# Performance work log

Hardware: AMD Instinct MI355X
Metric: run time of the kernel (lower is better)

## Reference

```python
import jax, jax.numpy as jnp
import numpy as np

N_NODES = 250000
N_EDGES = 5000000


def setup_inputs() -> dict:
    key = jax.random.key(0)
    k1, k2, k3, k4, k5, k6 = jax.random.split(key, 6)
    x = jax.random.normal(k1, (N_NODES, 1), dtype=jnp.float32)
    edge_index = jax.random.randint(k2, (2, N_EDGES), 0, N_NODES, dtype=jnp.int64)
    # Glorot-style small weights like PyG GCNConv init
    W1 = jax.random.normal(k3, (1, 16), dtype=jnp.float32) * (1.0 / np.sqrt(1 + 16))
    b1 = jnp.zeros((16,), dtype=jnp.float32)
    W2 = jax.random.normal(k4, (16, 2), dtype=jnp.float32) * (1.0 / np.sqrt(16 + 2))
    b2 = jnp.zeros((2,), dtype=jnp.float32)
    return {"x": x, "edge_index": edge_index, "W1": W1, "b1": b1, "W2": W2, "b2": b2}


def _gcn_conv(x, row, col, W, b, n_nodes):
    """PyG GCNConv: x' = D^{-1/2} (A + I) D^{-1/2} (x W) + b.

    row = source nodes, col = target nodes (messages flow row -> col).
    Self-loops are assumed already appended to row/col.
    """
    h = x @ W  # [N, out]
    ones = jnp.ones(row.shape[0], dtype=h.dtype)
    deg = jax.ops.segment_sum(ones, col, num_segments=n_nodes)  # in-degree incl. self-loop
    dinv = jnp.where(deg > 0, jax.lax.rsqrt(deg), 0.0)
    norm = dinv[row] * dinv[col]  # [E+N]
    msg = h[row] * norm[:, None]  # gather + scale  [E+N, out]
    out = jax.ops.segment_sum(msg, col, num_segments=n_nodes)  # scatter-add
    return out + b


def reference(x, edge_index, W1, b1, W2, b2):
    n = x.shape[0]
    loop = jnp.arange(n, dtype=edge_index.dtype)
    row = jnp.concatenate([edge_index[0], loop])
    col = jnp.concatenate([edge_index[1], loop])
    h = _gcn_conv(x, row, col, W1, b1, n)
    h = jax.nn.relu(h)
    # F.dropout(training=False) at inference -> identity
    h = _gcn_conv(h, row, col, W2, b2, n)
    return jax.nn.softmax(h, axis=1)
```

## Files before the change

kernel.cpp:

```cpp
#include <hip/hip_runtime.h>

#define ST 512
#define PT 24
#define EPB (ST * PT)
#define CSHIFT 10
#define CMASK 1023u
#define CW 1024
#define NCMAX 255
#define CAP 24576


__global__ void k_init(unsigned* __restrict__ gcur, int NC) {
    for (int b = threadIdx.x; b < NC; b += blockDim.x)
        gcur[b] = (unsigned)b * CAP;
}

__global__ __launch_bounds__(ST) void k_sortk(const int* __restrict__ row,
                                              const int* __restrict__ col,
                                              unsigned* __restrict__ gcur,
                                              unsigned* __restrict__ pack1,
                                              int E, int NC) {
    __shared__ unsigned loff[NCMAX + 2];
    __shared__ unsigned gbase[NCMAX + 1];
    __shared__ unsigned cur[NCMAX + 1];
    __shared__ unsigned staging[EPB];

    const int t = threadIdx.x;
    for (int i = t; i <= NC; i += ST) loff[i] = 0;
    __syncthreads();

    const int base = blockIdx.x * EPB;
    int c[PT];

#pragma unroll
    for (int k = 0; k < PT / 4; ++k) {
        int e = base + (k * ST + t) * 4;
        int4 cc;
        if (e + 3 < E) {
            cc = *reinterpret_cast<const int4*>(col + e);
        } else {
            cc.x = (e     < E) ? col[e]     : -1;
            cc.y = (e + 1 < E) ? col[e + 1] : -1;
            cc.z = (e + 2 < E) ? col[e + 2] : -1;
            cc.w = (e + 3 < E) ? col[e + 3] : -1;
        }
        c[4 * k] = cc.x; c[4 * k + 1] = cc.y; c[4 * k + 2] = cc.z; c[4 * k + 3] = cc.w;
    }
#pragma unroll
    for (int k = 0; k < PT; ++k)
        if (c[k] >= 0) atomicAdd(&loff[((unsigned)c[k] >> CSHIFT) + 1], 1u);
    __syncthreads();

    if (t < 64) {
        unsigned v[4];
        unsigned ls = 0;
#pragma unroll
        for (int k = 0; k < 4; ++k) {
            int idx = t * 4 + k;
            v[k] = (idx <= NC) ? loff[idx] : 0;
            ls += v[k];
        }
        unsigned sc = ls;
#pragma unroll
        for (int d = 1; d < 64; d <<= 1) {
            unsigned n = __shfl_up(sc, d, 64);
            if (t >= d) sc += n;
        }
        unsigned run = sc - ls;
#pragma unroll
        for (int k = 0; k < 4; ++k) {
            int idx = t * 4 + k;
            run += v[k];
            if (idx <= NC) loff[idx] = run;
        }
    }
    __syncthreads();

    if (t < NC) {
        unsigned cb = loff[t + 1] - loff[t];
        gbase[t] = atomicAdd(&gcur[t], cb);
        cur[t] = loff[t];
    }
    __syncthreads();

#pragma unroll
    for (int k = 0; k < PT / 4; ++k) {
        int e = base + (k * ST + t) * 4;
        int4 rr = make_int4(0, 0, 0, 0);
        if (e + 3 < E) {
            rr = *reinterpret_cast<const int4*>(row + e);
        } else {
            rr.x = (e     < E) ? row[e]     : 0;
            rr.y = (e + 1 < E) ? row[e + 1] : 0;
            rr.z = (e + 2 < E) ? row[e + 2] : 0;
            rr.w = (e + 3 < E) ? row[e + 3] : 0;
        }
        int rl[4] = {rr.x, rr.y, rr.z, rr.w};
#pragma unroll
        for (int j = 0; j < 4; ++j) {
            int cc = c[4 * k + j];
            if (cc >= 0) {
                unsigned b = (unsigned)cc >> CSHIFT;
                unsigned p = atomicAdd(&cur[b], 1u);
                staging[p] = ((unsigned)rl[j] << CSHIFT) | ((unsigned)cc & CMASK);
            }
        }
    }
    __syncthreads();

    const int wave = t >> 6;
    const int lane = t & 63;
    for (int b = wave; b < NC; b += ST / 64) {
        unsigned lo = loff[b];
        unsigned hi = loff[b + 1];
        unsigned gb = gbase[b];
        unsigned lim = (unsigned)(b + 1) * CAP;
        for (unsigned i = lo + lane; i < hi; i += 64) {
            unsigned pos = gb + (i - lo);
            if (pos < lim)
                pack1[pos] = staging[i];
        }
    }
}


__global__ __launch_bounds__(CW) void k_degk(const unsigned* __restrict__ pack1,
                                             const unsigned* __restrict__ gcur,
                                             const float* __restrict__ x,
                                             float* __restrict__ dinv, float* __restrict__ xs,
                                             int N) {
    __shared__ unsigned dcnt[CW];
    const int b = blockIdx.x;
    const int t = threadIdx.x;
    dcnt[t] = 0;
    __syncthreads();
    unsigned s0 = (unsigned)b * CAP;
    unsigned s1 = min(gcur[b], s0 + (unsigned)CAP);
    unsigned n4 = (s1 - s0) >> 2;
    for (unsigned i = t; i < n4; i += CW) {
        uint4 p = reinterpret_cast<const uint4*>(pack1 + s0)[i];
        atomicAdd(&dcnt[p.x & CMASK], 1u);
        atomicAdd(&dcnt[p.y & CMASK], 1u);
        atomicAdd(&dcnt[p.z & CMASK], 1u);
        atomicAdd(&dcnt[p.w & CMASK], 1u);
    }
    unsigned i = s0 + (n4 << 2) + t;
    if (i < s1) atomicAdd(&dcnt[pack1[i] & CMASK], 1u);
    __syncthreads();
    int v = (b << CSHIFT) + t;
    if (v < N) {
        float di = rsqrtf((float)dcnt[t] + 1.0f);
        dinv[v] = di;
        xs[v] = di * x[v];
    }
}

__global__ __launch_bounds__(CW) void k_l1k(const unsigned* __restrict__ pack1,
                                            const unsigned* __restrict__ gcur,
                                            const float* __restrict__ xs,
                                            const float* __restrict__ dinv,
                                            const float* __restrict__ W1,
                                            const float* __restrict__ b1,
                                            const float* __restrict__ W2,
                                            float* __restrict__ gs, int N) {
    __shared__ float acc[CW];
    const int b = blockIdx.x;
    const int t = threadIdx.x;
    acc[t] = 0.0f;
    __syncthreads();
    unsigned s0 = (unsigned)b * CAP;
    unsigned s1 = min(gcur[b], s0 + (unsigned)CAP);
    unsigned n4 = (s1 - s0) >> 2;
    for (unsigned i = t; i < n4; i += CW) {
        uint4 p = reinterpret_cast<const uint4*>(pack1 + s0)[i];
        float v0 = xs[p.x >> CSHIFT];
        float v1 = xs[p.y >> CSHIFT];
        float v2 = xs[p.z >> CSHIFT];
        float v3 = xs[p.w >> CSHIFT];
        atomicAdd(&acc[p.x & CMASK], v0);
        atomicAdd(&acc[p.y & CMASK], v1);
        atomicAdd(&acc[p.z & CMASK], v2);
        atomicAdd(&acc[p.w & CMASK], v3);
    }
    unsigned i = s0 + (n4 << 2) + t;
    if (i < s1) {
        unsigned p = pack1[i];
        atomicAdd(&acc[p & CMASK], xs[p >> CSHIFT]);
    }
    __syncthreads();
    int v = (b << CSHIFT) + t;
    if (v < N) {
        float di = dinv[v];
        float tt = di * (acc[t] + xs[v]);
        float g = 0.0f;
#pragma unroll
        for (int jj = 0; jj < 16; ++jj) {
            float y = fmaxf(fmaf(W1[jj], tt, b1[jj]), 0.0f);
            g = fmaf(W2[2 * jj] - W2[2 * jj + 1], y, g);
        }
        gs[v] = di * g;
    }
}

__global__ __launch_bounds__(CW) void k_l2k(const unsigned* __restrict__ pack1,
                                            const unsigned* __restrict__ gcur,
                                            const float* __restrict__ gs,
                                            const float* __restrict__ dinv,
                                            const float* __restrict__ b2,
                                            float* __restrict__ out, int N) {
    __shared__ float acc[CW];
    const int b = blockIdx.x;
    const int t = threadIdx.x;
    acc[t] = 0.0f;
    __syncthreads();
    unsigned s0 = (unsigned)b * CAP;
    unsigned s1 = min(gcur[b], s0 + (unsigned)CAP);
    unsigned n4 = (s1 - s0) >> 2;
    for (unsigned i = t; i < n4; i += CW) {
        uint4 p = reinterpret_cast<const uint4*>(pack1 + s0)[i];
        float v0 = gs[p.x >> CSHIFT];
        float v1 = gs[p.y >> CSHIFT];
        float v2 = gs[p.z >> CSHIFT];
        float v3 = gs[p.w >> CSHIFT];
        atomicAdd(&acc[p.x & CMASK], v0);
        atomicAdd(&acc[p.y & CMASK], v1);
        atomicAdd(&acc[p.z & CMASK], v2);
        atomicAdd(&acc[p.w & CMASK], v3);
    }
    unsigned i = s0 + (n4 << 2) + t;
    if (i < s1) {
        unsigned p = pack1[i];
        atomicAdd(&acc[p & CMASK], gs[p >> CSHIFT]);
    }
    __syncthreads();
    int v = (b << CSHIFT) + t;
    if (v < N) {
        float diff = dinv[v] * (acc[t] + gs[v]) + (b2[0] - b2[1]);
        float p0 = 1.0f / (1.0f + __expf(-diff));
        float2 o;
        o.x = p0;
        o.y = 1.0f - p0;
        reinterpret_cast<float2*>(out)[v] = o;
    }
}

__global__ void k_zero_f(float* __restrict__ p, int n) {
    int i = blockIdx.x * blockDim.x + threadIdx.x;
    int v = i * 4;
    if (v + 3 < n) {
        reinterpret_cast<float4*>(p + v)[0] = make_float4(0.f, 0.f, 0.f, 0.f);
    } else {
        for (; v < n; ++v) p[v] = 0.0f;
    }
}
__global__ void k_deg_f(const int* __restrict__ col, float* __restrict__ deg, int E) {
    int i = blockIdx.x * blockDim.x + threadIdx.x;
    int e = i * 4;
    if (e + 3 < E) {
        int4 c = reinterpret_cast<const int4*>(col + e)[0];
        atomicAdd(deg + c.x, 1.0f); atomicAdd(deg + c.y, 1.0f);
        atomicAdd(deg + c.z, 1.0f); atomicAdd(deg + c.w, 1.0f);
    } else {
        for (; e < E; ++e) atomicAdd(deg + col[e], 1.0f);
    }
}
__global__ void k_node1_f(const float* __restrict__ x, float* __restrict__ degdinv,
                          float* __restrict__ xs, int N) {
    int v = blockIdx.x * blockDim.x + threadIdx.x;
    if (v < N) {
        float dinv = rsqrtf(degdinv[v] + 1.0f);
        degdinv[v] = dinv;
        xs[v] = dinv * x[v];
    }
}
__global__ void k_scat_f(const int* __restrict__ row, const int* __restrict__ col,
                         const float* __restrict__ src, float* __restrict__ acc, int E) {
    int i = blockIdx.x * blockDim.x + threadIdx.x;
    int e = i * 4;
    if (e + 3 < E) {
        int4 r = reinterpret_cast<const int4*>(row + e)[0];
        int4 c = reinterpret_cast<const int4*>(col + e)[0];
        float s0 = src[r.x], s1 = src[r.y], s2 = src[r.z], s3 = src[r.w];
        atomicAdd(acc + c.x, s0); atomicAdd(acc + c.y, s1);
        atomicAdd(acc + c.z, s2); atomicAdd(acc + c.w, s3);
    } else {
        for (; e < E; ++e) atomicAdd(acc + col[e], src[row[e]]);
    }
}
__global__ void k_mlp_f(const float* __restrict__ W1, const float* __restrict__ b1,
                        const float* __restrict__ W2, const float* __restrict__ dinv,
                        float* __restrict__ acc, float* __restrict__ xsgs, int N) {
    int v = blockIdx.x * blockDim.x + threadIdx.x;
    if (v < N) {
        float di = dinv[v];
        float t = di * (acc[v] + xsgs[v]);
        float g = 0.0f;
#pragma unroll
        for (int j = 0; j < 16; ++j) {
            float y = fmaxf(fmaf(W1[j], t, b1[j]), 0.0f);
            g = fmaf(W2[2 * j] - W2[2 * j + 1], y, g);
        }
        xsgs[v] = di * g;
        acc[v] = 0.0f;
    }
}
__global__ void k_out_f(const float* __restrict__ b2, const float* __restrict__ dinv,
                        const float* __restrict__ acc, const float* __restrict__ gs,
                        float* __restrict__ out, int N) {
    int v = blockIdx.x * blockDim.x + threadIdx.x;
    if (v < N) {
        float diff = dinv[v] * (acc[v] + gs[v]) + (b2[0] - b2[1]);
        float p0 = 1.0f / (1.0f + __expf(-diff));
        float2 o; o.x = p0; o.y = 1.0f - p0;
        reinterpret_cast<float2*>(out)[v] = o;
    }
}

extern "C" void kernel_launch(void* const* d_in, const int* in_sizes, int n_in,
                              void* d_out, int out_size, void* d_ws, size_t ws_size,
                              hipStream_t stream) {
    const float* x  = (const float*)d_in[0];
    const int* edge = (const int*)d_in[1];
    const float* W1 = (const float*)d_in[2];
    const float* b1 = (const float*)d_in[3];
    const float* W2 = (const float*)d_in[4];
    const float* b2 = (const float*)d_in[5];
    float* out = (float*)d_out;

    const int N = in_sizes[0];
    const int E = in_sizes[1] / 2;
    const int* row = edge;
    const int* col = edge + E;

    const int NC  = (N + CW - 1) >> CSHIFT;
    const int NBS = (E + EPB - 1) / EPB;

    const double mean = (double)E / NC;
    const double slack = mean + 8.0 * __builtin_sqrt(mean > 1.0 ? mean : 1.0);
    const size_t need = ((size_t)NC * CAP + NC) * 4 + (size_t)3 * N * 4;

    if (NC <= NCMAX && N < (1 << 22) && slack < CAP && ws_size >= need) {
        unsigned* pack1 = (unsigned*)d_ws;
        unsigned* gcur  = pack1 + (size_t)NC * CAP;
        float* dinv     = (float*)(gcur + NC);
        float* xs       = dinv + N;
        float* gs       = xs + N;

        k_init <<<1, 256, 0, stream>>>(gcur, NC);
        k_sortk<<<NBS, ST, 0, stream>>>(row, col, gcur, pack1, E, NC);
        k_degk <<<NC, CW, 0, stream>>>(pack1, gcur, x, dinv, xs, N);
        k_l1k  <<<NC, CW, 0, stream>>>(pack1, gcur, xs, dinv, W1, b1, W2, gs, N);
        k_l2k  <<<NC, CW, 0, stream>>>(pack1, gcur, gs, dinv, b2, out, N);
    } else {
        float* w0 = (float*)d_ws;
        float* w1 = w0 + N;
        float* w2 = w1 + N;
        const int nb = (N + 255) / 256;
        const int eb = ((E + 3) / 4 + 255) / 256;
        const int zb = ((2 * N + 3) / 4 + 255) / 256;
        k_zero_f <<<zb, 256, 0, stream>>>(w0, 2 * N);
        k_deg_f  <<<eb, 256, 0, stream>>>(col, w0, E);
        k_node1_f<<<nb, 256, 0, stream>>>(x, w0, w2, N);
        k_scat_f <<<eb, 256, 0, stream>>>(row, col, w2, w1, E);
        k_mlp_f  <<<nb, 256, 0, stream>>>(W1, b1, W2, w0, w1, w2, N);
        k_scat_f <<<eb, 256, 0, stream>>>(row, col, w2, w1, E);
        k_out_f  <<<nb, 256, 0, stream>>>(b2, w0, w1, w2, out, N);
    }
}
```

Baseline: 174.6 us.

## Sub-bucket edges by source slice and gather node values from LDS

Each destination bucket is split into 8 sub-buckets keyed by source-node slice. The sort kernel uses wave ballots to rank elements and reserve positions with per-sub-bucket atomics. The layer kernels then stage each 32K-node slice of xs/gs into 128KB of dynamic LDS and gather from shared memory instead of doing random global loads. The cost is extra ballot work in the sort, eight serial slice loads per block, scalar instead of uint4 edge loads, and much lower occupancy from the large LDS footprint.

```diff
diff --git a/kernel.cpp b/kernel.cpp
--- a/kernel.cpp
+++ b/kernel.cpp
@@ -1,18 +1,23 @@
 #include <hip/hip_runtime.h>
 
 #define ST 512
-#define PT 24
+#define PT 20
 #define EPB (ST * PT)
 #define CSHIFT 10
 #define CMASK 1023u
 #define CW 1024
 #define NCMAX 255
-#define CAP 24576
-
-
-__global__ void k_init(unsigned* __restrict__ gcur, int NC) {
-    for (int b = threadIdx.x; b < NC; b += blockDim.x)
-        gcur[b] = (unsigned)b * CAP;
+#define NS 8
+#define SSHIFT 15
+#define SMASK 32767u
+#define SLICE 32768
+#define SUBCAP 3072
+#define CAP (NS * SUBCAP)
+
+
+__global__ void k_init(unsigned* __restrict__ gcur, int NSB) {
+    for (int i = threadIdx.x; i < NSB; i += blockDim.x)
+        gcur[i] = (unsigned)i * SUBCAP;
 }
 
 __global__ __launch_bounds__(ST) void k_sortk(const int* __restrict__ row,
@@ -21,7 +26,6 @@
                                               unsigned* __restrict__ pack1,
                                               int E, int NC) {
     __shared__ unsigned loff[NCMAX + 2];
-    __shared__ unsigned gbase[NCMAX + 1];
     __shared__ unsigned cur[NCMAX + 1];
     __shared__ unsigned staging[EPB];
 
@@ -76,11 +80,7 @@
     }
     __syncthreads();
 
-    if (t < NC) {
-        unsigned cb = loff[t + 1] - loff[t];
-        gbase[t] = atomicAdd(&gcur[t], cb);
-        cur[t] = loff[t];
-    }
+    if (t < NC) cur[t] = loff[t];
     __syncthreads();
 
 #pragma unroll
@@ -110,15 +110,33 @@
 
     const int wave = t >> 6;
     const int lane = t & 63;
+    const unsigned long long lanemask_lt = (lane == 0) ? 0ull : ((~0ull) >> (64 - lane));
     for (int b = wave; b < NC; b += ST / 64) {
         unsigned lo = loff[b];
         unsigned hi = loff[b + 1];
-        unsigned gb = gbase[b];
-        unsigned lim = (unsigned)(b + 1) * CAP;
-        for (unsigned i = lo + lane; i < hi; i += 64) {
-            unsigned pos = gb + (i - lo);
-            if (pos < lim)
-                pack1[pos] = staging[i];
+        for (unsigned i0 = lo; i0 < hi; i0 += 64) {
+            unsigned i = i0 + lane;
+            bool valid = i < hi;
+            unsigned p = valid ? staging[i] : 0u;
+            unsigned sl = p >> (CSHIFT + SSHIFT);
+            unsigned long long mymask = 0;
+            unsigned cnt8 = 0;
+#pragma unroll
+            for (int s = 0; s < NS; ++s) {
+                unsigned long long m = __ballot(valid && sl == (unsigned)s);
+                if (valid && sl == (unsigned)s) mymask = m;
+                if (lane == s) cnt8 = (unsigned)__popcll(m);
+            }
+            unsigned rbase = 0;
+            if (lane < NS && cnt8)
+                rbase = atomicAdd(&gcur[b * NS + lane], cnt8);
+            unsigned mybase = __shfl(rbase, (int)sl, 64);
+            if (valid) {
+                unsigned rank = (unsigned)__popcll(mymask & lanemask_lt);
+                unsigned pos = mybase + rank;
+                if (pos < ((unsigned)b * NS + sl + 1u) * (unsigned)SUBCAP)
+                    pack1[pos] = p;
+            }
         }
     }
 }
@@ -134,18 +152,13 @@
     const int t = threadIdx.x;
     dcnt[t] = 0;
     __syncthreads();
-    unsigned s0 = (unsigned)b * CAP;
-    unsigned s1 = min(gcur[b], s0 + (unsigned)CAP);
-    unsigned n4 = (s1 - s0) >> 2;
-    for (unsigned i = t; i < n4; i += CW) {
-        uint4 p = reinterpret_cast<const uint4*>(pack1 + s0)[i];
-        atomicAdd(&dcnt[p.x & CMASK], 1u);
-        atomicAdd(&dcnt[p.y & CMASK], 1u);
-        atomicAdd(&dcnt[p.z & CMASK], 1u);
-        atomicAdd(&dcnt[p.w & CMASK], 1u);
-    }
-    unsigned i = s0 + (n4 << 2) + t;
-    if (i < s1) atomicAdd(&dcnt[pack1[i] & CMASK], 1u);
+    for (int s = 0; s < NS; ++s) {
+        unsigned sb = (unsigned)b * NS + s;
+        unsigned sbase = sb * SUBCAP;
+        unsigned cnt = min(gcur[sb] - sbase, (unsigned)SUBCAP);
+        for (unsigned i = t; i < cnt; i += CW)
+            atomicAdd(&dcnt[pack1[sbase + i] & CMASK], 1u);
+    }
     __syncthreads();
     int v = (b << CSHIFT) + t;
     if (v < N) {
@@ -154,6 +167,7 @@
         xs[v] = di * x[v];
     }
 }
+
 
 __global__ __launch_bounds__(CW) void k_l1k(const unsigned* __restrict__ pack1,
                                             const unsigned* __restrict__ gcur,
@@ -163,31 +177,31 @@
                                             const float* __restrict__ b1,
                                             const float* __restrict__ W2,
                                             float* __restrict__ gs, int N) {
+    extern __shared__ float sbuf[];
     __shared__ float acc[CW];
     const int b = blockIdx.x;
     const int t = threadIdx.x;
     acc[t] = 0.0f;
-    __syncthreads();
-    unsigned s0 = (unsigned)b * CAP;
-    unsigned s1 = min(gcur[b], s0 + (unsigned)CAP);
-    unsigned n4 = (s1 - s0) >> 2;
-    for (unsigned i = t; i < n4; i += CW) {
-        uint4 p = reinterpret_cast<const uint4*>(pack1 + s0)[i];
-        float v0 = xs[p.x >> CSHIFT];
-        float v1 = xs[p.y >> CSHIFT];
-        float v2 = xs[p.z >> CSHIFT];
-        float v3 = xs[p.w >> CSHIFT];
-        atomicAdd(&acc[p.x & CMASK], v0);
-        atomicAdd(&acc[p.y & CMASK], v1);
-        atomicAdd(&acc[p.z & CMASK], v2);
-        atomicAdd(&acc[p.w & CMASK], v3);
-    }
-    unsigned i = s0 + (n4 << 2) + t;
-    if (i < s1) {
-        unsigned p = pack1[i];
-        atomicAdd(&acc[p & CMASK], xs[p >> CSHIFT]);
-    }
-    __syncthreads();
+    const int n4 = N >> 2;
+    for (int s = 0; s < NS; ++s) {
+        const float4* x4 = reinterpret_cast<const float4*>(xs) + s * (SLICE / 4);
+        float4* b4 = reinterpret_cast<float4*>(sbuf);
+        const int lim = n4 - s * (SLICE / 4);
+#pragma unroll
+        for (int k = 0; k < SLICE / 4 / CW; ++k) {
+            int j = k * CW + t;
+            b4[j] = (j < lim) ? x4[j] : make_float4(0.f, 0.f, 0.f, 0.f);
+        }
+        __syncthreads();
+        unsigned sb = (unsigned)b * NS + s;
+        unsigned sbase = sb * SUBCAP;
+        unsigned cnt = min(gcur[sb] - sbase, (unsigned)SUBCAP);
+        for (unsigned i = t; i < cnt; i += CW) {
+            unsigned p = pack1[sbase + i];
+            atomicAdd(&acc[p & CMASK], sbuf[(p >> CSHIFT) & SMASK]);
+        }
+        __syncthreads();
+    }
     int v = (b << CSHIFT) + t;
     if (v < N) {
         float di = dinv[v];
@@ -208,31 +222,31 @@
                                             const float* __restrict__ dinv,
                                             const float* __restrict__ b2,
                                             float* __restrict__ out, int N) {
+    extern __shared__ float sbuf[];
     __shared__ float acc[CW];
     const int b = blockIdx.x;
     const int t = threadIdx.x;
     acc[t] = 0.0f;
-    __syncthreads();
-    unsigned s0 = (unsigned)b * CAP;
-    unsigned s1 = min(gcur[b], s0 + (unsigned)CAP);
-    unsigned n4 = (s1 - s0) >> 2;
-    for (unsigned i = t; i < n4; i += CW) {
-        uint4 p = reinterpret_cast<const uint4*>(pack1 + s0)[i];
-        float v0 = gs[p.x >> CSHIFT];
-        float v1 = gs[p.y >> CSHIFT];
-        float v2 = gs[p.z >> CSHIFT];
-        float v3 = gs[p.w >> CSHIFT];
-        atomicAdd(&acc[p.x & CMASK], v0);
-        atomicAdd(&acc[p.y & CMASK], v1);
-        atomicAdd(&acc[p.z & CMASK], v2);
-        atomicAdd(&acc[p.w & CMASK], v3);
-    }
-    unsigned i = s0 + (n4 << 2) + t;
-    if (i < s1) {
-        unsigned p = pack1[i];
-        atomicAdd(&acc[p & CMASK], gs[p >> CSHIFT]);
-    }
-    __syncthreads();
+    const int n4 = N >> 2;
+    for (int s = 0; s < NS; ++s) {
+        const float4* g4 = reinterpret_cast<const float4*>(gs) + s * (SLICE / 4);
+        float4* b4 = reinterpret_cast<float4*>(sbuf);
+        const int lim = n4 - s * (SLICE / 4);
+#pragma unroll
+        for (int k = 0; k < SLICE / 4 / CW; ++k) {
+            int j = k * CW + t;
+            b4[j] = (j < lim) ? g4[j] : make_float4(0.f, 0.f, 0.f, 0.f);
+        }
+        __syncthreads();
+        unsigned sb = (unsigned)b * NS + s;
+        unsigned sbase = sb * SUBCAP;
+        unsigned cnt = min(gcur[sb] - sbase, (unsigned)SUBCAP);
+        for (unsigned i = t; i < cnt; i += CW) {
+            unsigned p = pack1[sbase + i];
+            atomicAdd(&acc[p & CMASK], sbuf[(p >> CSHIFT) & SMASK]);
+        }
+        __syncthreads();
+    }
     int v = (b << CSHIFT) + t;
     if (v < N) {
         float diff = dinv[v] * (acc[t] + gs[v]) + (b2[0] - b2[1]);
@@ -333,24 +347,35 @@
     const int* col = edge + E;
 
     const int NC  = (N + CW - 1) >> CSHIFT;
+    const int NSB = NC * NS;
     const int NBS = (E + EPB - 1) / EPB;
 
-    const double mean = (double)E / NC;
-    const double slack = mean + 8.0 * __builtin_sqrt(mean > 1.0 ? mean : 1.0);
-    const size_t need = ((size_t)NC * CAP + NC) * 4 + (size_t)3 * N * 4;
-
-    if (NC <= NCMAX && N < (1 << 22) && slack < CAP && ws_size >= need) {
+    const double mean_sb = (double)E / ((double)NC * NS);
+    const double slack = mean_sb + 8.0 * __builtin_sqrt(mean_sb > 1.0 ? mean_sb : 1.0);
+    const size_t need = ((size_t)NC * CAP + NSB) * 4 + (size_t)3 * N * 4;
+
+    if (NC <= NCMAX && N <= NS * SLICE && (N & 3) == 0 && slack < SUBCAP &&
+        ws_size >= need) {
         unsigned* pack1 = (unsigned*)d_ws;
         unsigned* gcur  = pack1 + (size_t)NC * CAP;
-        float* dinv     = (float*)(gcur + NC);
+        float* dinv     = (float*)(gcur + NSB);
         float* xs       = dinv + N;
         float* gs       = xs + N;
 
-        k_init <<<1, 256, 0, stream>>>(gcur, NC);
+        static bool attr_done = false;
+        if (!attr_done) {
+            hipFuncSetAttribute((const void*)k_l1k,
+                                hipFuncAttributeMaxDynamicSharedMemorySize, SLICE * 4);
+            hipFuncSetAttribute((const void*)k_l2k,
+                                hipFuncAttributeMaxDynamicSharedMemorySize, SLICE * 4);
+            attr_done = true;
+        }
+
+        k_init <<<1, 256, 0, stream>>>(gcur, NSB);
         k_sortk<<<NBS, ST, 0, stream>>>(row, col, gcur, pack1, E, NC);
         k_degk <<<NC, CW, 0, stream>>>(pack1, gcur, x, dinv, xs, N);
-        k_l1k  <<<NC, CW, 0, stream>>>(pack1, gcur, xs, dinv, W1, b1, W2, gs, N);
-        k_l2k  <<<NC, CW, 0, stream>>>(pack1, gcur, gs, dinv, b2, out, N);
+        k_l1k  <<<NC, CW, SLICE * 4, stream>>>(pack1, gcur, xs, dinv, W1, b1, W2, gs, N);
+        k_l2k  <<<NC, CW, SLICE * 4, stream>>>(pack1, gcur, gs, dinv, b2, out, N);
     } else {
         float* w0 = (float*)d_ws;
         float* w1 = w0 + N;
```

New measurement: 275.1 us. 57.5% more time.

## Sub-sort buckets by source tile and gather layer features from LDS tiles

Applied to the files above, without the earlier changes.

Adds a per-destination-bucket counting sort, k_subk, that orders packed edges by 1024-node source tile. It records per-tile offsets in a new boff array and also computes degrees. Layer kernels now have each wave stage a 1024-node source tile of xs/gs into LDS, then gather from LDS instead of doing random global loads. The bucket cursor becomes a relative offset reset by a memset rather than an init kernel, and the sort's per-thread edge count drops. The cost is an extra read/write pass over the packed edges and a full 4 KB tile load for each non-empty (dst, src) tile pair, which may hold only a few dozen edges.

```diff
diff --git a/kernel.cpp b/kernel.cpp
--- a/kernel.cpp
+++ b/kernel.cpp
@@ -1,19 +1,15 @@
 #include <hip/hip_runtime.h>
 
 #define ST 512
-#define PT 24
+#define PT 20
 #define EPB (ST * PT)
 #define CSHIFT 10
 #define CMASK 1023u
 #define CW 1024
 #define NCMAX 255
 #define CAP 24576
-
-
-__global__ void k_init(unsigned* __restrict__ gcur, int NC) {
-    for (int b = threadIdx.x; b < NC; b += blockDim.x)
-        gcur[b] = (unsigned)b * CAP;
-}
+#define NWAVE (CW / 64)
+
 
 __global__ __launch_bounds__(ST) void k_sortk(const int* __restrict__ row,
                                               const int* __restrict__ col,
@@ -114,39 +110,78 @@
         unsigned lo = loff[b];
         unsigned hi = loff[b + 1];
         unsigned gb = gbase[b];
-        unsigned lim = (unsigned)(b + 1) * CAP;
         for (unsigned i = lo + lane; i < hi; i += 64) {
-            unsigned pos = gb + (i - lo);
-            if (pos < lim)
-                pack1[pos] = staging[i];
-        }
-    }
-}
-
-
-__global__ __launch_bounds__(CW) void k_degk(const unsigned* __restrict__ pack1,
+            unsigned off = gb + (i - lo);
+            if (off < CAP)
+                pack1[(unsigned)b * CAP + off] = staging[i];
+        }
+    }
+}
+
+
+__global__ __launch_bounds__(CW) void k_subk(unsigned* __restrict__ pack1,
                                              const unsigned* __restrict__ gcur,
                                              const float* __restrict__ x,
-                                             float* __restrict__ dinv, float* __restrict__ xs,
-                                             int N) {
+                                             float* __restrict__ dinv,
+                                             float* __restrict__ xs,
+                                             unsigned* __restrict__ boff,
+                                             int N, int NC) {
+    extern __shared__ unsigned sstage[];
+    __shared__ unsigned loff[NCMAX + 2];
+    __shared__ unsigned cur[NCMAX + 1];
     __shared__ unsigned dcnt[CW];
     const int b = blockIdx.x;
     const int t = threadIdx.x;
     dcnt[t] = 0;
-    __syncthreads();
-    unsigned s0 = (unsigned)b * CAP;
-    unsigned s1 = min(gcur[b], s0 + (unsigned)CAP);
-    unsigned n4 = (s1 - s0) >> 2;
-    for (unsigned i = t; i < n4; i += CW) {
-        uint4 p = reinterpret_cast<const uint4*>(pack1 + s0)[i];
-        atomicAdd(&dcnt[p.x & CMASK], 1u);
-        atomicAdd(&dcnt[p.y & CMASK], 1u);
-        atomicAdd(&dcnt[p.z & CMASK], 1u);
-        atomicAdd(&dcnt[p.w & CMASK], 1u);
-    }
-    unsigned i = s0 + (n4 << 2) + t;
-    if (i < s1) atomicAdd(&dcnt[pack1[i] & CMASK], 1u);
-    __syncthreads();
+    for (int i = t; i <= NC; i += CW) loff[i] = 0;
+    __syncthreads();
+
+    const unsigned s0 = (unsigned)b * CAP;
+    const unsigned cnt = min(gcur[b], (unsigned)CAP);
+
+    for (unsigned i = t; i < cnt; i += CW)
+        atomicAdd(&loff[(pack1[s0 + i] >> (CSHIFT + 10)) + 1], 1u);
+    __syncthreads();
+
+    if (t < 64) {
+        unsigned v[4];
+        unsigned ls = 0;
+#pragma unroll
+        for (int k = 0; k < 4; ++k) {
+            int idx = t * 4 + k;
+            v[k] = (idx <= NC) ? loff[idx] : 0;
+            ls += v[k];
+        }
+        unsigned sc = ls;
+#pragma unroll
+        for (int d = 1; d < 64; d <<= 1) {
+            unsigned n = __shfl_up(sc, d, 64);
+            if (t >= d) sc += n;
+        }
+        unsigned run = sc - ls;
+#pragma unroll
+        for (int k = 0; k < 4; ++k) {
+            int idx = t * 4 + k;
+            run += v[k];
+            if (idx <= NC) loff[idx] = run;
+        }
+    }
+    __syncthreads();
+    if (t <= NC) boff[(size_t)b * (NC + 1) + t] = loff[t];
+    if (t < NC) cur[t] = loff[t];
+    __syncthreads();
+
+    for (unsigned i = t; i < cnt; i += CW) {
+        unsigned p = pack1[s0 + i];
+        unsigned tile = p >> (CSHIFT + 10);
+        unsigned pos = atomicAdd(&cur[tile], 1u);
+        sstage[pos] = p;
+        atomicAdd(&dcnt[p & CMASK], 1u);
+    }
+    __syncthreads();
+
+    for (unsigned i = t; i < cnt; i += CW)
+        pack1[s0 + i] = sstage[i];
     int v = (b << CSHIFT) + t;
     if (v < N) {
         float di = rsqrtf((float)dcnt[t] + 1.0f);
@@ -155,37 +190,48 @@
     }
 }
 
+
 __global__ __launch_bounds__(CW) void k_l1k(const unsigned* __restrict__ pack1,
-                                            const unsigned* __restrict__ gcur,
+                                            const unsigned* __restrict__ boff,
                                             const float* __restrict__ xs,
                                             const float* __restrict__ dinv,
                                             const float* __restrict__ W1,
                                             const float* __restrict__ b1,
                                             const float* __restrict__ W2,
-                                            float* __restrict__ gs, int N) {
+                                            float* __restrict__ gs, int N, int NC) {
+    extern __shared__ float xtile[];
     __shared__ float acc[CW];
+    __shared__ unsigned bo[NCMAX + 2];
     const int b = blockIdx.x;
     const int t = threadIdx.x;
+    const int w = t >> 6;
+    const int lane = t & 63;
     acc[t] = 0.0f;
-    __syncthreads();
-    unsigned s0 = (unsigned)b * CAP;
-    unsigned s1 = min(gcur[b], s0 + (unsigned)CAP);
-    unsigned n4 = (s1 - s0) >> 2;
-    for (unsigned i = t; i < n4; i += CW) {
-        uint4 p = reinterpret_cast<const uint4*>(pack1 + s0)[i];
-        float v0 = xs[p.x >> CSHIFT];
-        float v1 = xs[p.y >> CSHIFT];
-        float v2 = xs[p.z >> CSHIFT];
-        float v3 = xs[p.w >> CSHIFT];
-        atomicAdd(&acc[p.x & CMASK], v0);
-        atomicAdd(&acc[p.y & CMASK], v1);
-        atomicAdd(&acc[p.z & CMASK], v2);
-        atomicAdd(&acc[p.w & CMASK], v3);
-    }
-    unsigned i = s0 + (n4 << 2) + t;
-    if (i < s1) {
-        unsigned p = pack1[i];
-        atomicAdd(&acc[p & CMASK], xs[p >> CSHIFT]);
+    if (t <= NC) bo[t] = boff[(size_t)b * (NC + 1) + t];
+    __syncthreads();
+
+    const unsigned s0 = (unsigned)b * CAP;
+    const int n44 = N >> 2;
+    const float4* x4 = reinterpret_cast<const float4*>(xs);
+    float4* tile4 = reinterpret_cast<float4*>(xtile + (w << 10));
+
+    for (int s = w; s < NC; s += NWAVE) {
+        unsigned off0 = bo[s];
+        unsigned off1 = bo[s + 1];
+        if (off0 == off1) continue;
+        int base4 = s << 8;
+#pragma unroll
+        for (int k = 0; k < 4; ++k) {
+            int q = lane + (k << 6);
+            int idx = base4 + q;
+            tile4[q] = (idx < n44) ? x4[idx] : make_float4(0.f, 0.f, 0.f, 0.f);
+        }
+        asm volatile("s_waitcnt lgkmcnt(0) vmcnt(0)" ::: "memory");
+        for (unsigned i = off0 + lane; i < off1; i += 64) {
+            unsigned p = pack1[s0 + i];
+            float val = xtile[(w << 10) | ((p >> CSHIFT) & CMASK)];
+            atomicAdd(&acc[p & CMASK], val);
+        }
     }
     __syncthreads();
     int v = (b << CSHIFT) + t;
@@ -203,34 +249,44 @@
 }
 
 __global__ __launch_bounds__(CW) void k_l2k(const unsigned* __restrict__ pack1,
-                                            const unsigned* __restrict__ gcur,
+                                            const unsigned* __restrict__ boff,
                                             const float* __restrict__ gs,
                                             const float* __restrict__ dinv,
                                             const float* __restrict__ b2,
-                                            float* __restrict__ out, int N) {
+                                            float* __restrict__ out, int N, int NC) {
+    extern __shared__ float xtile[];
     __shared__ float acc[CW];
+    __shared__ unsigned bo[NCMAX + 2];
     const int b = blockIdx.x;
     const int t = threadIdx.x;
+    const int w = t >> 6;
+    const int lane = t & 63;
     acc[t] = 0.0f;
-    __syncthreads();
-    unsigned s0 = (unsigned)b * CAP;
-    unsigned s1 = min(gcur[b], s0 + (unsigned)CAP);
-    unsigned n4 = (s1 - s0) >> 2;
-    for (unsigned i = t; i < n4; i += CW) {
-        uint4 p = reinterpret_cast<const uint4*>(pack1 + s0)[i];
-        float v0 = gs[p.x >> CSHIFT];
-        float v1 = gs[p.y >> CSHIFT];
-        float v2 = gs[p.z >> CSHIFT];
-        float v3 = gs[p.w >> CSHIFT];
-        atomicAdd(&acc[p.x & CMASK], v0);
-        atomicAdd(&acc[p.y & CMASK], v1);
-        atomicAdd(&acc[p.z & CMASK], v2);
-        atomicAdd(&acc[p.w & CMASK], v3);
-    }
-    unsigned i = s0 + (n4 << 2) + t;
-    if (i < s1) {
-        unsigned p = pack1[i];
-        atomicAdd(&acc[p & CMASK], gs[p >> CSHIFT]);
+    if (t <= NC) bo[t] = boff[(size_t)b * (NC + 1) + t];
+    __syncthreads();
+
+    const unsigned s0 = (unsigned)b * CAP;
+    const int n44 = N >> 2;
+    const float4* g4 = reinterpret_cast<const float4*>(gs);
+    float4* tile4 = reinterpret_cast<float4*>(xtile + (w << 10));
+
+    for (int s = w; s < NC; s += NWAVE) {
+        unsigned off0 = bo[s];
+        unsigned off1 = bo[s + 1];
+        if (off0 == off1) continue;
+        int base4 = s << 8;
+#pragma unroll
+        for (int k = 0; k < 4; ++k) {
+            int q = lane + (k << 6);
+            int idx = base4 + q;
+            tile4[q] = (idx < n44) ? g4[idx] : make_float4(0.f, 0.f, 0.f, 0.f);
+        }
+        asm volatile("s_waitcnt lgkmcnt(0) vmcnt(0)" ::: "memory");
+        for (unsigned i = off0 + lane; i < off1; i += 64) {
+            unsigned p = pack1[s0 + i];
+            float val = xtile[(w << 10) | ((p >> CSHIFT) & CMASK)];
+            atomicAdd(&acc[p & CMASK], val);
+        }
     }
     __syncthreads();
     int v = (b << CSHIFT) + t;
@@ -337,20 +393,38 @@
 
     const double mean = (double)E / NC;
     const double slack = mean + 8.0 * __builtin_sqrt(mean > 1.0 ? mean : 1.0);
-    const size_t need = ((size_t)NC * CAP + NC) * 4 + (size_t)3 * N * 4;
-
-    if (NC <= NCMAX && N < (1 << 22) && slack < CAP && ws_size >= need) {
+    const size_t need = ((size_t)NC * CAP + NC + (size_t)NC * (NC + 1)) * 4 +
+                        (size_t)3 * N * 4;
+
+    if (NC <= NCMAX && N < (1 << 22) && (N & 3) == 0 && slack < CAP &&
+        ws_size >= need) {
         unsigned* pack1 = (unsigned*)d_ws;
         unsigned* gcur  = pack1 + (size_t)NC * CAP;
-        float* dinv     = (float*)(gcur + NC);
+        unsigned* boff  = gcur + NC;
+        float* dinv     = (float*)(boff + (size_t)NC * (NC + 1));
         float* xs       = dinv + N;
         float* gs       = xs + N;
 
-        k_init <<<1, 256, 0, stream>>>(gcur, NC);
+        static bool attr_done = false;
+        if (!attr_done) {
+            hipFuncSetAttribute((const void*)k_subk,
+                                hipFuncAttributeMaxDynamicSharedMemorySize, CAP * 4);
+            hipFuncSetAttribute((const void*)k_l1k,
+                                hipFuncAttributeMaxDynamicSharedMemorySize,
+                                NWAVE * 1024 * 4);
+            hipFuncSetAttribute((const void*)k_l2k,
+                                hipFuncAttributeMaxDynamicSharedMemorySize,
+                                NWAVE * 1024 * 4);
+            attr_done = true;
+        }
+
+        hipMemsetAsync(gcur, 0, (size_t)NC * sizeof(unsigned), stream);
         k_sortk<<<NBS, ST, 0, stream>>>(row, col, gcur, pack1, E, NC);
-        k_degk <<<NC, CW, 0, stream>>>(pack1, gcur, x, dinv, xs, N);
-        k_l1k  <<<NC, CW, 0, stream>>>(pack1, gcur, xs, dinv, W1, b1, W2, gs, N);
-        k_l2k  <<<NC, CW, 0, stream>>>(pack1, gcur, gs, dinv, b2, out, N);
+        k_subk <<<NC, CW, CAP * 4, stream>>>(pack1, gcur, x, dinv, xs, boff, N, NC);
+        k_l1k  <<<NC, CW, NWAVE * 1024 * 4, stream>>>(pack1, boff, xs, dinv, W1, b1,
+                                                      W2, gs, N, NC);
+        k_l2k  <<<NC, CW, NWAVE * 1024 * 4, stream>>>(pack1, boff, gs, dinv, b2, out,
+                                                      N, NC);
     } else {
         float* w0 = (float*)d_ws;
         float* w1 = w0 + N;
```

New measurement: 250.0 us. 43.2% more time.

## Halve destination bucket width to double per-bucket blocks and parallelism

Applied to the files above, without the earlier changes.

Destination nodes are bucketed into 512-wide groups instead of 1024-wide, which doubles the number of bucket blocks (about 489 instead of 245) in the degree and aggregation kernels, with 1024 threads per block. The sort kernel now handles up to 511 buckets with a wider per-thread scan, processes 20 edges per thread, and stores offsets relative to each bucket. The init kernel is replaced by a memset of the bucket counters. The aim is better CU occupancy on the aggregation kernels. The cost is more bucket atomics and more scattered small writes in the sort, plus more LDS atomic contention on a 512-entry accumulator.

```diff
diff --git a/kernel.cpp b/kernel.cpp
--- a/kernel.cpp
+++ b/kernel.cpp
@@ -1,32 +1,28 @@
 #include <hip/hip_runtime.h>
 
 #define ST 512
-#define PT 24
+#define PT 20
 #define EPB (ST * PT)
-#define CSHIFT 10
-#define CMASK 1023u
-#define CW 1024
-#define NCMAX 255
-#define CAP 24576
-
-
-__global__ void k_init(unsigned* __restrict__ gcur, int NC) {
-    for (int b = threadIdx.x; b < NC; b += blockDim.x)
-        gcur[b] = (unsigned)b * CAP;
-}
+#define BSHIFT 9
+#define BMASK 511u
+#define BW 512
+#define GT 1024
+#define NBMAX 511
+#define CAP 12288
+
 
 __global__ __launch_bounds__(ST) void k_sortk(const int* __restrict__ row,
                                               const int* __restrict__ col,
                                               unsigned* __restrict__ gcur,
                                               unsigned* __restrict__ pack1,
-                                              int E, int NC) {
-    __shared__ unsigned loff[NCMAX + 2];
-    __shared__ unsigned gbase[NCMAX + 1];
-    __shared__ unsigned cur[NCMAX + 1];
+                                              int E, int NB) {
+    __shared__ unsigned loff[NBMAX + 2];
+    __shared__ unsigned gbase[NBMAX + 1];
+    __shared__ unsigned cur[NBMAX + 1];
     __shared__ unsigned staging[EPB];
 
     const int t = threadIdx.x;
-    for (int i = t; i <= NC; i += ST) loff[i] = 0;
+    for (int i = t; i <= NB; i += ST) loff[i] = 0;
     __syncthreads();
 
     const int base = blockIdx.x * EPB;
@@ -48,16 +44,16 @@
     }
 #pragma unroll
     for (int k = 0; k < PT; ++k)
-        if (c[k] >= 0) atomicAdd(&loff[((unsigned)c[k] >> CSHIFT) + 1], 1u);
+        if (c[k] >= 0) atomicAdd(&loff[((unsigned)c[k] >> BSHIFT) + 1], 1u);
     __syncthreads();
 
     if (t < 64) {
-        unsigned v[4];
+        unsigned v[8];
         unsigned ls = 0;
 #pragma unroll
-        for (int k = 0; k < 4; ++k) {
-            int idx = t * 4 + k;
-            v[k] = (idx <= NC) ? loff[idx] : 0;
+        for (int k = 0; k < 8; ++k) {
+            int idx = t * 8 + k;
+            v[k] = (idx <= NB) ? loff[idx] : 0;
             ls += v[k];
         }
         unsigned sc = ls;
@@ -68,15 +64,15 @@
         }
         unsigned run = sc - ls;
 #pragma unroll
-        for (int k = 0; k < 4; ++k) {
-            int idx = t * 4 + k;
+        for (int k = 0; k < 8; ++k) {
+            int idx = t * 8 + k;
             run += v[k];
-            if (idx <= NC) loff[idx] = run;
-        }
-    }
-    __syncthreads();
-
-    if (t < NC) {
+            if (idx <= NB) loff[idx] = run;
+        }
+    }
+    __syncthreads();
+
+    if (t < NB) {
         unsigned cb = loff[t + 1] - loff[t];
         gbase[t] = atomicAdd(&gcur[t], cb);
         cur[t] = loff[t];
@@ -100,9 +96,9 @@
         for (int j = 0; j < 4; ++j) {
             int cc = c[4 * k + j];
             if (cc >= 0) {
-                unsigned b = (unsigned)cc >> CSHIFT;
+                unsigned b = (unsigned)cc >> BSHIFT;
                 unsigned p = atomicAdd(&cur[b], 1u);
-                staging[p] = ((unsigned)rl[j] << CSHIFT) | ((unsigned)cc & CMASK);
+                staging[p] = ((unsigned)rl[j] << BSHIFT) | ((unsigned)cc & BMASK);
             }
         }
     }
@@ -110,52 +106,56 @@
 
     const int wave = t >> 6;
     const int lane = t & 63;
-    for (int b = wave; b < NC; b += ST / 64) {
+    for (int b = wave; b < NB; b += ST / 64) {
         unsigned lo = loff[b];
         unsigned hi = loff[b + 1];
         unsigned gb = gbase[b];
-        unsigned lim = (unsigned)(b + 1) * CAP;
         for (unsigned i = lo + lane; i < hi; i += 64) {
-            unsigned pos = gb + (i - lo);
-            if (pos < lim)
-                pack1[pos] = staging[i];
-        }
-    }
-}
-
-
-__global__ __launch_bounds__(CW) void k_degk(const unsigned* __restrict__ pack1,
+            unsigned off = gb + (i - lo);
+            if (off < CAP)
+                pack1[(unsigned)b * CAP + off] = staging[i];
+        }
+    }
+}
+
+
+__global__ __launch_bounds__(GT) void k_degk(const unsigned* __restrict__ pack1,
                                              const unsigned* __restrict__ gcur,
                                              const float* __restrict__ x,
                                              float* __restrict__ dinv, float* __restrict__ xs,
                                              int N) {
-    __shared__ unsigned dcnt[CW];
+    __shared__ unsigned dcnt[BW];
     const int b = blockIdx.x;
     const int t = threadIdx.x;
-    dcnt[t] = 0;
-    __syncthreads();
+    if (t < BW) dcnt[t] = 0;
+    __syncthreads();
+    unsigned cnt = gcur[b];
+    if (cnt > CAP) cnt = CAP;
     unsigned s0 = (unsigned)b * CAP;
-    unsigned s1 = min(gcur[b], s0 + (unsigned)CAP);
-    unsigned n4 = (s1 - s0) >> 2;
-    for (unsigned i = t; i < n4; i += CW) {
-        uint4 p = reinterpret_cast<const uint4*>(pack1 + s0)[i];
-        atomicAdd(&dcnt[p.x & CMASK], 1u);
-        atomicAdd(&dcnt[p.y & CMASK], 1u);
-        atomicAdd(&dcnt[p.z & CMASK], 1u);
-        atomicAdd(&dcnt[p.w & CMASK], 1u);
+    unsigned n4 = cnt >> 2;
+    const uint4* pk = reinterpret_cast<const uint4*>(pack1 + s0);
+    for (unsigned i = t; i < n4; i += GT) {
+        uint4 p = pk[i];
+        atomicAdd(&dcnt[p.x & BMASK], 1u);
+        atomicAdd(&dcnt[p.y & BMASK], 1u);
+        atomicAdd(&dcnt[p.z & BMASK], 1u);
+        atomicAdd(&dcnt[p.w & BMASK], 1u);
     }
     unsigned i = s0 + (n4 << 2) + t;
-    if (i < s1) atomicAdd(&dcnt[pack1[i] & CMASK], 1u);
-    __syncthreads();
-    int v = (b << CSHIFT) + t;
-    if (v < N) {
-        float di = rsqrtf((float)dcnt[t] + 1.0f);
-        dinv[v] = di;
-        xs[v] = di * x[v];
-    }
-}
-
-__global__ __launch_bounds__(CW) void k_l1k(const unsigned* __restrict__ pack1,
+    if (i < s0 + cnt) atomicAdd(&dcnt[pack1[i] & BMASK], 1u);
+    __syncthreads();
+    if (t < BW) {
+        int v = (b << BSHIFT) + t;
+        if (v < N) {
+            float di = rsqrtf((float)dcnt[t] + 1.0f);
+            dinv[v] = di;
+            xs[v] = di * x[v];
+        }
+    }
+}
+
+
+__global__ __launch_bounds__(GT) void k_l1k(const unsigned* __restrict__ pack1,
                                             const unsigned* __restrict__ gcur,
                                             const float* __restrict__ xs,
                                             const float* __restrict__ dinv,
@@ -163,84 +163,94 @@
                                             const float* __restrict__ b1,
                                             const float* __restrict__ W2,
                                             float* __restrict__ gs, int N) {
-    __shared__ float acc[CW];
+    __shared__ float acc[BW];
     const int b = blockIdx.x;
     const int t = threadIdx.x;
-    acc[t] = 0.0f;
-    __syncthreads();
+    if (t < BW) acc[t] = 0.0f;
+    __syncthreads();
+    unsigned cnt = gcur[b];
+    if (cnt > CAP) cnt = CAP;
     unsigned s0 = (unsigned)b * CAP;
-    unsigned s1 = min(gcur[b], s0 + (unsigned)CAP);
-    unsigned n4 = (s1 - s0) >> 2;
-    for (unsigned i = t; i < n4; i += CW) {
-        uint4 p = reinterpret_cast<const uint4*>(pack1 + s0)[i];
-        float v0 = xs[p.x >> CSHIFT];
-        float v1 = xs[p.y >> CSHIFT];
-        float v2 = xs[p.z >> CSHIFT];
-        float v3 = xs[p.w >> CSHIFT];
-        atomicAdd(&acc[p.x & CMASK], v0);
-        atomicAdd(&acc[p.y & CMASK], v1);
-        atomicAdd(&acc[p.z & CMASK], v2);
-        atomicAdd(&acc[p.w & CMASK], v3);
-    }
-    unsigned i = s0 + (n4 << 2) + t;
-    if (i < s1) {
-        unsigned p = pack1[i];
-        atomicAdd(&acc[p & CMASK], xs[p >> CSHIFT]);
-    }
-    __syncthreads();
-    int v = (b << CSHIFT) + t;
-    if (v < N) {
-        float di = dinv[v];
-        float tt = di * (acc[t] + xs[v]);
-        float g = 0.0f;
-#pragma unroll
-        for (int jj = 0; jj < 16; ++jj) {
-            float y = fmaxf(fmaf(W1[jj], tt, b1[jj]), 0.0f);
-            g = fmaf(W2[2 * jj] - W2[2 * jj + 1], y, g);
-        }
-        gs[v] = di * g;
-    }
-}
-
-__global__ __launch_bounds__(CW) void k_l2k(const unsigned* __restrict__ pack1,
+    unsigned s1 = s0 + cnt;
+    unsigned n4 = cnt >> 2;
+    const uint4* pk = reinterpret_cast<const uint4*>(pack1 + s0);
+    for (unsigned i = t; i < n4; i += GT) {
+        uint4 p = pk[i];
+        float a0 = xs[p.x >> BSHIFT];
+        float a1 = xs[p.y >> BSHIFT];
+        float a2 = xs[p.z >> BSHIFT];
+        float a3 = xs[p.w >> BSHIFT];
+        atomicAdd(&acc[p.x & BMASK], a0);
+        atomicAdd(&acc[p.y & BMASK], a1);
+        atomicAdd(&acc[p.z & BMASK], a2);
+        atomicAdd(&acc[p.w & BMASK], a3);
+    }
+    unsigned j = s0 + (n4 << 2) + t;
+    if (j < s1) {
+        unsigned p = pack1[j];
+        atomicAdd(&acc[p & BMASK], xs[p >> BSHIFT]);
+    }
+    __syncthreads();
+    if (t < BW) {
+        int v = (b << BSHIFT) + t;
+        if (v < N) {
+            float di = dinv[v];
+            float tt = di * (acc[t] + xs[v]);
+            float g = 0.0f;
+#pragma unroll
+            for (int jj = 0; jj < 16; ++jj) {
+                float y = fmaxf(fmaf(W1[jj], tt, b1[jj]), 0.0f);
+                g = fmaf(W2[2 * jj] - W2[2 * jj + 1], y, g);
+            }
+            gs[v] = di * g;
+        }
+    }
+}
+
+__global__ __launch_bounds__(GT) void k_l2k(const unsigned* __restrict__ pack1,
                                             const unsigned* __restrict__ gcur,
                                             const float* __restrict__ gs,
                                             const float* __restrict__ dinv,
                                             const float* __restrict__ b2,
                                             float* __restrict__ out, int N) {
-    __shared__ float acc[CW];
+    __shared__ float acc[BW];
     const int b = blockIdx.x;
     const int t = threadIdx.x;
-    acc[t] = 0.0f;
-    __syncthreads();
+    if (t < BW) acc[t] = 0.0f;
+    __syncthreads();
+    unsigned cnt = gcur[b];
+    if (cnt > CAP) cnt = CAP;
     unsigned s0 = (unsigned)b * CAP;
-    unsigned s1 = min(gcur[b], s0 + (unsigned)CAP);
-    unsigned n4 = (s1 - s0) >> 2;
-    for (unsigned i = t; i < n4; i += CW) {
-        uint4 p = reinterpret_cast<const uint4*>(pack1 + s0)[i];
-        float v0 = gs[p.x >> CSHIFT];
-        float v1 = gs[p.y >> CSHIFT];
-        float v2 = gs[p.z >> CSHIFT];
-        float v3 = gs[p.w >> CSHIFT];
-        atomicAdd(&acc[p.x & CMASK], v0);
-        atomicAdd(&acc[p.y & CMASK], v1);
-        atomicAdd(&acc[p.z & CMASK], v2);
-        atomicAdd(&acc[p.w & CMASK], v3);
-    }
-    unsigned i = s0 + (n4 << 2) + t;
-    if (i < s1) {
-        unsigned p = pack1[i];
-        atomicAdd(&acc[p & CMASK], gs[p >> CSHIFT]);
-    }
-    __syncthreads();
-    int v = (b << CSHIFT) + t;
-    if (v < N) {
-        float diff = dinv[v] * (acc[t] + gs[v]) + (b2[0] - b2[1]);
-        float p0 = 1.0f / (1.0f + __expf(-diff));
-        float2 o;
-        o.x = p0;
-        o.y = 1.0f - p0;
-        reinterpret_cast<float2*>(out)[v] = o;
+    unsigned s1 = s0 + cnt;
+    unsigned n4 = cnt >> 2;
+    const uint4* pk = reinterpret_cast<const uint4*>(pack1 + s0);
+    for (unsigned i = t; i < n4; i += GT) {
+        uint4 p = pk[i];
+        float a0 = gs[p.x >> BSHIFT];
+        float a1 = gs[p.y >> BSHIFT];
+        float a2 = gs[p.z >> BSHIFT];
+        float a3 = gs[p.w >> BSHIFT];
+        atomicAdd(&acc[p.x & BMASK], a0);
+        atomicAdd(&acc[p.y & BMASK], a1);
+        atomicAdd(&acc[p.z & BMASK], a2);
+        atomicAdd(&acc[p.w & BMASK], a3);
+    }
+    unsigned j = s0 + (n4 << 2) + t;
+    if (j < s1) {
+        unsigned p = pack1[j];
+        atomicAdd(&acc[p & BMASK], gs[p >> BSHIFT]);
+    }
+    __syncthreads();
+    if (t < BW) {
+        int v = (b << BSHIFT) + t;
+        if (v < N) {
+            float diff = dinv[v] * (acc[t] + gs[v]) + (b2[0] - b2[1]);
+            float p0 = 1.0f / (1.0f + __expf(-diff));
+            float2 o;
+            o.x = p0;
+            o.y = 1.0f - p0;
+            reinterpret_cast<float2*>(out)[v] = o;
+        }
     }
 }
 
@@ -332,25 +342,25 @@
     const int* row = edge;
     const int* col = edge + E;
 
-    const int NC  = (N + CW - 1) >> CSHIFT;
+    const int NB  = (N + BW - 1) >> BSHIFT;
     const int NBS = (E + EPB - 1) / EPB;
 
-    const double mean = (double)E / NC;
+    const double mean = (double)E / NB;
     const double slack = mean + 8.0 * __builtin_sqrt(mean > 1.0 ? mean : 1.0);
-    const size_t need = ((size_t)NC * CAP + NC) * 4 + (size_t)3 * N * 4;
-
-    if (NC <= NCMAX && N < (1 << 22) && slack < CAP && ws_size >= need) {
+    const size_t need = ((size_t)NB * CAP + NB) * 4 + (size_t)3 * N * 4;
+
+    if (NB <= NBMAX && N < (1 << 23) && slack < CAP && ws_size >= need) {
         unsigned* pack1 = (unsigned*)d_ws;
-        unsigned* gcur  = pack1 + (size_t)NC * CAP;
-        float* dinv     = (float*)(gcur + NC);
+        unsigned* gcur  = pack1 + (size_t)NB * CAP;
+        float* dinv     = (float*)(gcur + NB);
         float* xs       = dinv + N;
         float* gs       = xs + N;
 
-        k_init <<<1, 256, 0, stream>>>(gcur, NC);
-        k_sortk<<<NBS, ST, 0, stream>>>(row, col, gcur, pack1, E, NC);
-        k_degk <<<NC, CW, 0, stream>>>(pack1, gcur, x, dinv, xs, N);
-        k_l1k  <<<NC, CW, 0, stream>>>(pack1, gcur, xs, dinv, W1, b1, W2, gs, N);
-        k_l2k  <<<NC, CW, 0, stream>>>(pack1, gcur, gs, dinv, b2, out, N);
+        hipMemsetAsync(gcur, 0, (size_t)NB * sizeof(unsigned), stream);
+        k_sortk<<<NBS, ST, 0, stream>>>(row, col, gcur, pack1, E, NB);
+        k_degk <<<NB, GT, 0, stream>>>(pack1, gcur, x, dinv, xs, N);
+        k_l1k  <<<NB, GT, 0, stream>>>(pack1, gcur, xs, dinv, W1, b1, W2, gs, N);
+        k_l2k  <<<NB, GT, 0, stream>>>(pack1, gcur, gs, dinv, b2, out, N);
     } else {
         float* w0 = (float*)d_ws;
         float* w1 = w0 + N;
```

Result: slower. 181.5 us (+3.9%).
